# Kernel tuning notes

Measured on AMD Instinct MI355X. Metric: run time of the kernel, lower is better.

## Reference

```python
import jax
import jax.numpy as jnp
import numpy as np

IN_FEATS = 784
HIDDEN_DIM = 1024
BATCH = 1024


def setup_inputs() -> dict:
    key = jax.random.key(0)
    k_px, k_W, k_c, k_V, k_b = jax.random.split(key, 5)
    pixels = jax.random.uniform(k_px, (BATCH, IN_FEATS), dtype=jnp.float32)
    W = jax.random.normal(k_W, (HIDDEN_DIM, IN_FEATS), dtype=jnp.float32)
    c = jax.random.normal(k_c, (HIDDEN_DIM,), dtype=jnp.float32)
    V = jax.random.normal(k_V, (IN_FEATS, HIDDEN_DIM), dtype=jnp.float32)
    b = jax.random.normal(k_b, (IN_FEATS,), dtype=jnp.float32)
    return {"pixels": pixels, "W": W, "c": c, "V": V, "b": b}


def reference(pixels, W, c, V, b):
    # pixels: [B, D]; W: [H, D]; c: [H]; V: [D, H]; b: [D]
    B = pixels.shape[0]
    a0 = jnp.broadcast_to(c[None, :], (B, c.shape[0]))  # [B, H]

    def step(a, inp):
        w_col, v_row, b_i, x_i = inp  # [H], [H], [], [B]
        h = jax.nn.sigmoid(a)                     # [B, H]
        pred_i = b_i + h @ v_row                  # [B]
        a_next = a + w_col[None, :] * x_i[:, None]  # rank-1 accumulator update
        return a_next, pred_i

    xs = (W.T, V, b, pixels.T)  # each leading dim D (scan over visible units)
    _, preds = jax.lax.scan(step, a0, xs)  # preds: [D, B]
    return preds.T  # [B, D]
```

## Files before the change

### kernel.cpp

```cpp
#include <hip/hip_runtime.h>

#define B_ 1024
#define D_ 784
#define H_ 1024
#define BH_ (B_ * H_)
#define LOG2E 1.4426950408889634f


__global__ __launch_bounds__(256) void transpose_scale_W(const float* __restrict__ W,
                                                         float* __restrict__ Wt) {
    __shared__ float t[32][33];
    int i0 = blockIdx.x * 32;
    int h0 = blockIdx.y * 32;
    int tx = threadIdx.x & 31, ty = threadIdx.x >> 5;
#pragma unroll
    for (int j = 0; j < 4; ++j) {
        int h = h0 + ty + j * 8;
        int i = i0 + tx;
        float v = 0.f;
        if (i < D_) v = W[(size_t)h * D_ + i] * LOG2E;
        t[ty + j * 8][tx] = v;
    }
    __syncthreads();
#pragma unroll
    for (int j = 0; j < 4; ++j) {
        int i = i0 + ty + j * 8;
        int h = h0 + tx;
        if (i < D_) Wt[(size_t)i * H_ + h] = t[tx][ty + j * 8];
    }
}

__global__ __launch_bounds__(256) void prefix_gemm(const float* __restrict__ px,
                                                   const float* __restrict__ Wt,
                                                   const float* __restrict__ c,
                                                   float* __restrict__ A0) {
    __shared__ float xs[8][64];
    __shared__ float ws[8][64];
    const int t = threadIdx.x;
    const int b0 = blockIdx.x * 64, h0 = blockIdx.y * 64;
    const int tb = t >> 4, th = t & 15;

    float acc[4][4];
    float4 c4 = *(const float4*)(c + h0 + th * 4);
#pragma unroll
    for (int bi = 0; bi < 4; ++bi) {
        acc[bi][0] = c4.x * LOG2E; acc[bi][1] = c4.y * LOG2E;
        acc[bi][2] = c4.z * LOG2E; acc[bi][3] = c4.w * LOG2E;
    }
    const int xr = t >> 2, xc = (t & 3) * 2;

    for (int j0 = 0; j0 < 592; j0 += 8) {
        float2 xv = *(const float2*)(px + (size_t)(b0 + xr) * D_ + j0 + xc);
        float4 wv = make_float4(0, 0, 0, 0);
        if (t < 128) wv = *(const float4*)(Wt + (size_t)(j0 + (t >> 4)) * H_ + h0 + (t & 15) * 4);
        __syncthreads();
        xs[xc][xr] = xv.x; xs[xc + 1][xr] = xv.y;
        if (t < 128) *(float4*)&ws[t >> 4][(t & 15) * 4] = wv;
        __syncthreads();
#pragma unroll
        for (int jj = 0; jj < 8; ++jj) {
            float4 xb = *(float4*)&xs[jj][tb * 4];
            float4 wb = *(float4*)&ws[jj][th * 4];
            float xa[4] = {xb.x, xb.y, xb.z, xb.w};
            float wa[4] = {wb.x, wb.y, wb.z, wb.w};
#pragma unroll
            for (int bi = 0; bi < 4; ++bi)
#pragma unroll
                for (int hi = 0; hi < 4; ++hi)
                    acc[bi][hi] = fmaf(xa[bi], wa[hi], acc[bi][hi]);
        }
        int jend = j0 + 8;
        if (jend == 200 || jend == 400 || jend == 592) {
            int sidx = (jend == 200) ? 0 : (jend == 400) ? 1 : 2;
            float* dst = A0 + (size_t)sidx * BH_;
#pragma unroll
            for (int bi = 0; bi < 4; ++bi) {
                float4 o = make_float4(acc[bi][0], acc[bi][1], acc[bi][2], acc[bi][3]);
                *(float4*)(dst + (size_t)(b0 + tb * 4 + bi) * H_ + h0 + th * 4) = o;
            }
        }
    }
}

template <int CTRL>
__device__ __forceinline__ float dpp_add(float p) {
    int s = __builtin_amdgcn_update_dpp(0, __float_as_int(p), CTRL, 0xf, 0xf, true);
    return p + __int_as_float(s);
}
__device__ __forceinline__ float reduce_halves(float p) {
    p = dpp_add<0x111>(p);
    p = dpp_add<0x112>(p);
    p = dpp_add<0x114>(p);
    p = dpp_add<0x118>(p);
    p = dpp_add<0x142>(p);
    return p;
}

__global__ __launch_bounds__(256, 8) void nade_main(
    const float* __restrict__ px,
    const float* __restrict__ c,
    const float* __restrict__ V,
    const float* __restrict__ Wt,
    const float* __restrict__ A0,
    float* __restrict__ part)
{
    const int lane = threadIdx.x & 63;
    const int wid  = threadIdx.x >> 6;
    const int gw   = blockIdx.x * 4 + wid;
    const int s    = gw & 3;
    const int r2   = gw >> 2;
    const int hb   = r2 & 7;
    const int rp   = r2 >> 3;
    const int half = lane >> 5;
    const int row  = rp * 2 + half;
    const int h0   = hb * 128 + (lane & 31) * 4;

    int i0, i1;
    if      (s == 0) { i0 = 0;   i1 = 200; }
    else if (s == 1) { i0 = 200; i1 = 400; }
    else if (s == 2) { i0 = 400; i1 = 592; }
    else             { i0 = 592; i1 = 784; }

    float A[4];
    if (s == 0) {
        float4 a4 = *(const float4*)(c + h0);
        A[0] = a4.x * LOG2E; A[1] = a4.y * LOG2E; A[2] = a4.z * LOG2E; A[3] = a4.w * LOG2E;
    } else {
        float4 a4 = *(const float4*)(A0 + (size_t)(s - 1) * BH_ + (size_t)row * H_ + h0);
        A[0] = a4.x; A[1] = a4.y; A[2] = a4.z; A[3] = a4.w;
    }

    const float* vp = V  + h0;
    const float* wp = Wt + h0;
    const float* xp = px + (size_t)row * D_;
    float*       pp = part + ((size_t)hb * B_ + row) * D_;

    auto step = [&](const float4& v4, const float4& w4, float xi) -> float {
        float e0 = __builtin_amdgcn_exp2f(fminf(30.f, -A[0]));
        float e1 = __builtin_amdgcn_exp2f(fminf(30.f, -A[1]));
        float e2 = __builtin_amdgcn_exp2f(fminf(30.f, -A[2]));
        float e3 = __builtin_amdgcn_exp2f(fminf(30.f, -A[3]));
        float q0 = 1.f + e0, q1 = 1.f + e1, q2 = 1.f + e2, q3 = 1.f + e3;
        float q01 = q0 * q1, q23 = q2 * q3;
        float r = __builtin_amdgcn_rcpf(q01 * q23);
        float t0 = v4.x * q1; t0 = fmaf(v4.y, q0, t0);
        float t1 = v4.z * q3; t1 = fmaf(v4.w, q2, t1);
        float n  = t0 * q23;  n  = fmaf(t1, q01, n);
        A[0] = fmaf(w4.x, xi, A[0]);
        A[1] = fmaf(w4.y, xi, A[1]);
        A[2] = fmaf(w4.z, xi, A[2]);
        A[3] = fmaf(w4.w, xi, A[3]);
        return n * r;
    };

    float4 vv = *(const float4*)(vp + (size_t)i0 * H_);
    float4 ww = *(const float4*)(wp + (size_t)i0 * H_);
    float4 xq = *(const float4*)(xp + i0);

    for (int ib = i0; ib < i1; ib += 4) {
        int xbn = (ib + 4 < i1) ? (ib + 4) : i0;
        float4 xq_n = *(const float4*)(xp + xbn);
        float xa[4] = {xq.x, xq.y, xq.z, xq.w};
#pragma unroll
        for (int j = 0; j < 4; ++j) {
            int i  = ib + j;
            int ip = (i + 1 < i1) ? (i + 1) : (i1 - 1);
            float4 vn = *(const float4*)(vp + (size_t)ip * H_);
            float4 wn = *(const float4*)(wp + (size_t)ip * H_);
            float p = step(vv, ww, xa[j]);
            p = reduce_halves(p);
            if ((lane & 31) == 31) pp[i] = p;
            vv = vn; ww = wn;
        }
        xq = xq_n;
    }
}

__global__ __launch_bounds__(256) void reduce_out(const float* __restrict__ part,
                                                  const float* __restrict__ bias,
                                                  float* __restrict__ out) {
    int t = blockIdx.x * 256 + threadIdx.x;
    if (t >= B_ * (D_ / 4)) return;
    int row = t / (D_ / 4);
    int ic  = (t - row * (D_ / 4)) * 4;
    float4 acc = *(const float4*)(bias + ic);
    const float* p = part + (size_t)row * D_ + ic;
#pragma unroll
    for (int hb = 0; hb < 8; ++hb) {
        float4 v = *(const float4*)(p + (size_t)hb * B_ * D_);
        acc.x += v.x; acc.y += v.y; acc.z += v.z; acc.w += v.w;
    }
    *(float4*)(out + (size_t)row * D_ + ic) = acc;
}

extern "C" void kernel_launch(void* const* d_in, const int* in_sizes, int n_in,
                              void* d_out, int out_size, void* d_ws, size_t ws_size,
                              hipStream_t stream) {
    const float* px   = (const float*)d_in[0];
    const float* W    = (const float*)d_in[1];
    const float* c    = (const float*)d_in[2];
    const float* V    = (const float*)d_in[3];
    const float* bias = (const float*)d_in[4];
    float* out = (float*)d_out;

    float* Wt   = (float*)d_ws;
    float* A0   = Wt + (size_t)D_ * H_;
    float* part = A0 + (size_t)3 * BH_;

    transpose_scale_W<<<dim3((D_ + 31) / 32, H_ / 32), 256, 0, stream>>>(W, Wt);
    prefix_gemm<<<dim3(B_ / 64, H_ / 64), 256, 0, stream>>>(px, Wt, c, A0);

    nade_main<<<dim3(4096), 256, 0, stream>>>(px, c, V, Wt, A0, part);

    reduce_out<<<dim3((B_ * (D_ / 4) + 255) / 256), 256, 0, stream>>>(part, bias, out);
}
```

Baseline: 358.8 us.

## Interleave V and scaled W into one buffer; 8 hidden units per lane

The transpose kernel now writes V and LOG2E-scaled W^T interleaved per visible unit and 256-wide hidden block, so the main kernel reads both from one contiguous region. Each lane now handles 8 hidden units instead of 4. That halves the number of hidden blocks, which halves the partial-sum writes, the main grid size and the reduction work. The explicit one-step-ahead prefetch of V/W is dropped in favour of direct loads, and the four predictions are written as one float4. Doubling the accumulators per lane raises register pressure and halves the wave count, which may reduce latency hiding.

```diff
diff --git a/kernel.cpp b/kernel.cpp
--- a/kernel.cpp
+++ b/kernel.cpp
@@ -7,12 +7,20 @@
 #define LOG2E 1.4426950408889634f
 
 
-__global__ __launch_bounds__(256) void transpose_scale_W(const float* __restrict__ W,
-                                                         float* __restrict__ Wt) {
+__global__ __launch_bounds__(256) void build_vw(const float* __restrict__ V,
+                                                const float* __restrict__ W,
+                                                float* __restrict__ VW) {
     __shared__ float t[32][33];
     int i0 = blockIdx.x * 32;
     int h0 = blockIdx.y * 32;
     int tx = threadIdx.x & 31, ty = threadIdx.x >> 5;
+    int hb = h0 >> 8, hl = h0 & 255;
+#pragma unroll
+    for (int j = 0; j < 4; ++j) {
+        int i = i0 + ty + j * 8;
+        if (i < D_)
+            VW[((size_t)i * 4 + hb) * 512 + hl + tx] = V[(size_t)i * H_ + h0 + tx];
+    }
 #pragma unroll
     for (int j = 0; j < 4; ++j) {
         int h = h0 + ty + j * 8;
@@ -25,19 +33,20 @@
 #pragma unroll
     for (int j = 0; j < 4; ++j) {
         int i = i0 + ty + j * 8;
-        int h = h0 + tx;
-        if (i < D_) Wt[(size_t)i * H_ + h] = t[tx][ty + j * 8];
+        if (i < D_)
+            VW[((size_t)i * 4 + hb) * 512 + 256 + hl + tx] = t[tx][ty + j * 8];
     }
 }
 
 __global__ __launch_bounds__(256) void prefix_gemm(const float* __restrict__ px,
-                                                   const float* __restrict__ Wt,
+                                                   const float* __restrict__ VW,
                                                    const float* __restrict__ c,
                                                    float* __restrict__ A0) {
     __shared__ float xs[8][64];
     __shared__ float ws[8][64];
     const int t = threadIdx.x;
     const int b0 = blockIdx.x * 64, h0 = blockIdx.y * 64;
+    const int hbg = h0 >> 8, hlg = h0 & 255;
     const int tb = t >> 4, th = t & 15;
 
     float acc[4][4];
@@ -52,7 +61,8 @@
     for (int j0 = 0; j0 < 592; j0 += 8) {
         float2 xv = *(const float2*)(px + (size_t)(b0 + xr) * D_ + j0 + xc);
         float4 wv = make_float4(0, 0, 0, 0);
-        if (t < 128) wv = *(const float4*)(Wt + (size_t)(j0 + (t >> 4)) * H_ + h0 + (t & 15) * 4);
+        if (t < 128)
+            wv = *(const float4*)(VW + ((size_t)(j0 + (t >> 4)) * 4 + hbg) * 512 + 256 + hlg + (t & 15) * 4);
         __syncthreads();
         xs[xc][xr] = xv.x; xs[xc + 1][xr] = xv.y;
         if (t < 128) *(float4*)&ws[t >> 4][(t & 15) * 4] = wv;
@@ -99,8 +109,7 @@
 __global__ __launch_bounds__(256, 8) void nade_main(
     const float* __restrict__ px,
     const float* __restrict__ c,
-    const float* __restrict__ V,
-    const float* __restrict__ Wt,
+    const float* __restrict__ VW,
     const float* __restrict__ A0,
     float* __restrict__ part)
 {
@@ -108,71 +117,73 @@
     const int wid  = threadIdx.x >> 6;
     const int gw   = blockIdx.x * 4 + wid;
     const int s    = gw & 3;
-    const int r2   = gw >> 2;
-    const int hb   = r2 & 7;
-    const int rp   = r2 >> 3;
+    const int hb   = (gw >> 2) & 3;
+    const int rp   = gw >> 4;
     const int half = lane >> 5;
     const int row  = rp * 2 + half;
-    const int h0   = hb * 128 + (lane & 31) * 4;
-
-    int i0, i1;
-    if      (s == 0) { i0 = 0;   i1 = 200; }
-    else if (s == 1) { i0 = 200; i1 = 400; }
-    else if (s == 2) { i0 = 400; i1 = 592; }
-    else             { i0 = 592; i1 = 784; }
-
-    float A[4];
+    const int hl   = lane & 31;
+    const int h0   = hb * 256 + hl * 8;
+
+    int i0s, i1s;
+    if      (s == 0) { i0s = 0;   i1s = 200; }
+    else if (s == 1) { i0s = 200; i1s = 400; }
+    else if (s == 2) { i0s = 400; i1s = 592; }
+    else             { i0s = 592; i1s = 784; }
+
+    float A[8];
     if (s == 0) {
-        float4 a4 = *(const float4*)(c + h0);
-        A[0] = a4.x * LOG2E; A[1] = a4.y * LOG2E; A[2] = a4.z * LOG2E; A[3] = a4.w * LOG2E;
+        float4 a0 = *(const float4*)(c + h0);
+        float4 a1 = *(const float4*)(c + h0 + 4);
+        A[0] = a0.x * LOG2E; A[1] = a0.y * LOG2E; A[2] = a0.z * LOG2E; A[3] = a0.w * LOG2E;
+        A[4] = a1.x * LOG2E; A[5] = a1.y * LOG2E; A[6] = a1.z * LOG2E; A[7] = a1.w * LOG2E;
     } else {
-        float4 a4 = *(const float4*)(A0 + (size_t)(s - 1) * BH_ + (size_t)row * H_ + h0);
-        A[0] = a4.x; A[1] = a4.y; A[2] = a4.z; A[3] = a4.w;
-    }
-
-    const float* vp = V  + h0;
-    const float* wp = Wt + h0;
+        const float* ap = A0 + (size_t)(s - 1) * BH_ + (size_t)row * H_ + h0;
+        float4 a0 = *(const float4*)(ap);
+        float4 a1 = *(const float4*)(ap + 4);
+        A[0] = a0.x; A[1] = a0.y; A[2] = a0.z; A[3] = a0.w;
+        A[4] = a1.x; A[5] = a1.y; A[6] = a1.z; A[7] = a1.w;
+    }
+
     const float* xp = px + (size_t)row * D_;
     float*       pp = part + ((size_t)hb * B_ + row) * D_;
-
-    auto step = [&](const float4& v4, const float4& w4, float xi) -> float {
-        float e0 = __builtin_amdgcn_exp2f(fminf(30.f, -A[0]));
-        float e1 = __builtin_amdgcn_exp2f(fminf(30.f, -A[1]));
-        float e2 = __builtin_amdgcn_exp2f(fminf(30.f, -A[2]));
-        float e3 = __builtin_amdgcn_exp2f(fminf(30.f, -A[3]));
+    const float* vw = VW + ((size_t)i0s * 4 + hb) * 512 + hl * 8;
+
+    auto grp4 = [&A](const float4& v4, const float4& w4, float xi, int k0) -> float {
+        float e0 = __builtin_amdgcn_exp2f(fminf(30.f, -A[k0 + 0]));
+        float e1 = __builtin_amdgcn_exp2f(fminf(30.f, -A[k0 + 1]));
+        float e2 = __builtin_amdgcn_exp2f(fminf(30.f, -A[k0 + 2]));
+        float e3 = __builtin_amdgcn_exp2f(fminf(30.f, -A[k0 + 3]));
         float q0 = 1.f + e0, q1 = 1.f + e1, q2 = 1.f + e2, q3 = 1.f + e3;
         float q01 = q0 * q1, q23 = q2 * q3;
         float r = __builtin_amdgcn_rcpf(q01 * q23);
         float t0 = v4.x * q1; t0 = fmaf(v4.y, q0, t0);
         float t1 = v4.z * q3; t1 = fmaf(v4.w, q2, t1);
         float n  = t0 * q23;  n  = fmaf(t1, q01, n);
-        A[0] = fmaf(w4.x, xi, A[0]);
-        A[1] = fmaf(w4.y, xi, A[1]);
-        A[2] = fmaf(w4.z, xi, A[2]);
-        A[3] = fmaf(w4.w, xi, A[3]);
+        A[k0 + 0] = fmaf(w4.x, xi, A[k0 + 0]);
+        A[k0 + 1] = fmaf(w4.y, xi, A[k0 + 1]);
+        A[k0 + 2] = fmaf(w4.z, xi, A[k0 + 2]);
+        A[k0 + 3] = fmaf(w4.w, xi, A[k0 + 3]);
         return n * r;
     };
 
-    float4 vv = *(const float4*)(vp + (size_t)i0 * H_);
-    float4 ww = *(const float4*)(wp + (size_t)i0 * H_);
-    float4 xq = *(const float4*)(xp + i0);
-
-    for (int ib = i0; ib < i1; ib += 4) {
-        int xbn = (ib + 4 < i1) ? (ib + 4) : i0;
-        float4 xq_n = *(const float4*)(xp + xbn);
+    for (int ib = i0s; ib < i1s; ib += 4) {
+        float4 xq = *(const float4*)(xp + ib);
         float xa[4] = {xq.x, xq.y, xq.z, xq.w};
+        float pr[4];
 #pragma unroll
         for (int j = 0; j < 4; ++j) {
-            int i  = ib + j;
-            int ip = (i + 1 < i1) ? (i + 1) : (i1 - 1);
-            float4 vn = *(const float4*)(vp + (size_t)ip * H_);
-            float4 wn = *(const float4*)(wp + (size_t)ip * H_);
-            float p = step(vv, ww, xa[j]);
-            p = reduce_halves(p);
-            if ((lane & 31) == 31) pp[i] = p;
-            vv = vn; ww = wn;
-        }
-        xq = xq_n;
+            float4 v0 = *(const float4*)(vw + 0);
+            float4 v1 = *(const float4*)(vw + 4);
+            float4 w0 = *(const float4*)(vw + 256);
+            float4 w1 = *(const float4*)(vw + 260);
+            float p = grp4(v0, w0, xa[j], 0) + grp4(v1, w1, xa[j], 4);
+            pr[j] = reduce_halves(p);
+            vw += 2048;
+        }
+        if (hl == 31) {
+            float4 o = make_float4(pr[0], pr[1], pr[2], pr[3]);
+            *(float4*)(pp + ib) = o;
+        }
     }
 }
 
@@ -186,7 +197,7 @@
     float4 acc = *(const float4*)(bias + ic);
     const float* p = part + (size_t)row * D_ + ic;
 #pragma unroll
-    for (int hb = 0; hb < 8; ++hb) {
+    for (int hb = 0; hb < 4; ++hb) {
         float4 v = *(const float4*)(p + (size_t)hb * B_ * D_);
         acc.x += v.x; acc.y += v.y; acc.z += v.z; acc.w += v.w;
     }
@@ -203,14 +214,14 @@
     const float* bias = (const float*)d_in[4];
     float* out = (float*)d_out;
 
-    float* Wt   = (float*)d_ws;
-    float* A0   = Wt + (size_t)D_ * H_;
+    float* VW   = (float*)d_ws;
+    float* A0   = VW + (size_t)D_ * 2048;
     float* part = A0 + (size_t)3 * BH_;
 
-    transpose_scale_W<<<dim3((D_ + 31) / 32, H_ / 32), 256, 0, stream>>>(W, Wt);
-    prefix_gemm<<<dim3(B_ / 64, H_ / 64), 256, 0, stream>>>(px, Wt, c, A0);
-
-    nade_main<<<dim3(4096), 256, 0, stream>>>(px, c, V, Wt, A0, part);
+    build_vw<<<dim3((D_ + 31) / 32, H_ / 32), 256, 0, stream>>>(V, W, VW);
+    prefix_gemm<<<dim3(B_ / 64, H_ / 64), 256, 0, stream>>>(px, VW, c, A0);
+
+    nade_main<<<dim3(2048), 256, 0, stream>>>(px, c, VW, A0, part);
 
     reduce_out<<<dim3((B_ * (D_ / 4) + 255) / 256), 256, 0, stream>>>(part, bias, out);
 }
```

Result: faster. 348.0 us (-3.0%).
